# Kernel optimization log

Hardware: AMD Instinct MI355X
Metric: run time of the kernel (lower is better)

The kernel has to match this reference:

```python
import jax, jax.numpy as jnp
import numpy as np

N_HEADS = 8
N_LEVELS = 1
N_POINTS = 4
D_MODEL = 256
BATCH = 2
H0, W0 = 100, 150
LS = H0 * W0
LQ = 15000


def layer_norm(x, g, b, eps=1e-5):
    m = jnp.mean(x, -1, keepdims=True)
    v = jnp.var(x, -1, keepdims=True)
    return (x - m) * jax.lax.rsqrt(v + eps) * g + b


def bilinear_sample(v, Hl, Wl, loc):
    # v: [N, Hl*Wl, Hh, D] level features; loc in [0,1]: [N, Lq, Hh, P, 2] (x, y)
    Nb, _, Hh, D = v.shape
    Lq, P = loc.shape[1], loc.shape[3]
    x = loc[..., 0] * Wl - 0.5           # align_corners=False grid_sample convention
    y = loc[..., 1] * Hl - 0.5
    x0 = jnp.floor(x); y0 = jnp.floor(y)
    lx = (x - x0).transpose(0, 2, 1, 3)[..., None]   # [N,Hh,Lq,P,1]
    ly = (y - y0).transpose(0, 2, 1, 3)[..., None]
    x0i = x0.astype(jnp.int32); y0i = y0.astype(jnp.int32)
    vh = v.transpose(0, 2, 1, 3)                      # [N,Hh,Hl*Wl,D]

    def gather(xi, yi):
        valid = (xi >= 0) & (xi < Wl) & (yi >= 0) & (yi < Hl)   # zero padding
        idx = jnp.clip(yi, 0, Hl - 1) * Wl + jnp.clip(xi, 0, Wl - 1)
        idxf = idx.transpose(0, 2, 1, 3).reshape(Nb, Hh, Lq * P)
        g = jnp.take_along_axis(vh, idxf[..., None], axis=2).reshape(Nb, Hh, Lq, P, D)
        return g * valid.transpose(0, 2, 1, 3)[..., None]

    g00 = gather(x0i, y0i)
    g10 = gather(x0i + 1, y0i)
    g01 = gather(x0i, y0i + 1)
    g11 = gather(x0i + 1, y0i + 1)
    return (g00 * (1 - lx) * (1 - ly) + g10 * lx * (1 - ly)
            + g01 * (1 - lx) * ly + g11 * lx * ly)   # [N,Hh,Lq,P,D]


def ms_deform_attn(q, reference_points, src, shapes_np, starts_np, padding_mask,
                   W_val, b_val, W_off, b_off, W_attn, b_attn, W_out, b_out):
    Nb, Lq, C = q.shape
    Hh, D, L, P = N_HEADS, C // N_HEADS, N_LEVELS, N_POINTS
    value = src @ W_val + b_val
    value = jnp.where(padding_mask[..., None], 0.0, value).reshape(Nb, -1, Hh, D)
    offsets = (q @ W_off + b_off).reshape(Nb, Lq, Hh, L, P, 2)
    aw = jax.nn.softmax((q @ W_attn + b_attn).reshape(Nb, Lq, Hh, L * P), -1)
    aw = aw.reshape(Nb, Lq, Hh, L, P)
    # offset normalizer is (W, H) per level
    norm = jnp.asarray(shapes_np[:, ::-1].copy(), dtype=q.dtype)   # [L,2]
    loc = reference_points[:, :, None, :, None, :] + offsets / norm[None, None, None, :, None, :]
    out = 0.0
    for l in range(L):
        Hl, Wl = int(shapes_np[l, 0]), int(shapes_np[l, 1])
        s = int(starts_np[l])
        sampled = bilinear_sample(value[:, s:s + Hl * Wl], Hl, Wl, loc[:, :, :, l])
        out = out + jnp.sum(sampled * aw[:, :, :, l].transpose(0, 2, 1, 3)[..., None], axis=3)
    out = out.transpose(0, 2, 1, 3).reshape(Nb, Lq, C)
    return out @ W_out + b_out


def reference(tgt, query_pos, src_pos, tgt_spatial_shapes, reference_points,
              depth_reference_points, src, src_spatial_shapes, frame_start_index,
              src_padding_mask,
              W_dsa, b_dsa, g_nds, b_nds, W_off, b_off, W_attn, b_attn,
              W_val, b_val, W_out, b_out, W_csa, b_csa, g_n1, b_n1,
              W_ff, b_ff, g_n3, b_n3):
    ss = np.asarray(src_spatial_shapes)      # static level shapes
    starts = np.asarray(frame_start_index)
    # depth scale adaptation
    src_a = layer_norm(src @ W_dsa + b_dsa, g_nds, b_nds)
    q = tgt + query_pos
    tgt2 = ms_deform_attn(q, reference_points, src_a, ss, starts, src_padding_mask,
                          W_val, b_val, W_off, b_off, W_attn, b_attn, W_out, b_out)
    tgt2 = tgt2 @ W_csa + b_csa
    t = layer_norm(tgt + tgt2, g_n1, b_n1)
    # FFN: single linear d_model->d_model with exact GELU (per source code)
    ff = jax.nn.gelu(t @ W_ff + b_ff, approximate=False)
    return layer_norm(t + ff, g_n3, b_n3)


def setup_inputs() -> dict:
    key = jax.random.key(0)
    ks = jax.random.split(key, 24)
    C = D_MODEL
    Hh, L, P = N_HEADS, N_LEVELS, N_POINTS

    def lin(k, fin, fout, scale=None):
        s = (1.0 / np.sqrt(fin)) if scale is None else scale
        return (jax.random.normal(k, (fin, fout), jnp.float32) * s).astype(jnp.float32)

    inp = {}
    inp['tgt'] = jax.random.normal(ks[0], (BATCH, LQ, C), jnp.float32)
    inp['query_pos'] = 0.1 * jax.random.normal(ks[1], (BATCH, LQ, C), jnp.float32)
    inp['src_pos'] = 0.1 * jax.random.normal(ks[2], (BATCH, LS, C), jnp.float32)
    inp['tgt_spatial_shapes'] = jnp.array([[H0, W0]], jnp.int32)
    inp['reference_points'] = jax.random.uniform(ks[3], (BATCH, LQ, L, 2), jnp.float32)
    inp['depth_reference_points'] = jax.random.uniform(ks[4], (BATCH, LQ, 1, 2), jnp.float32)
    inp['src'] = jax.random.normal(ks[5], (BATCH, LS, C), jnp.float32)
    inp['src_spatial_shapes'] = jnp.array([[H0, W0]], jnp.int32)
    inp['frame_start_index'] = jnp.array([0], jnp.int32)
    inp['src_padding_mask'] = jnp.zeros((BATCH, LS), jnp.bool_)
    # parameters
    inp['W_dsa'] = lin(ks[6], C, C); inp['b_dsa'] = jnp.zeros((C,), jnp.float32)
    inp['g_nds'] = jnp.ones((C,), jnp.float32); inp['b_nds'] = jnp.zeros((C,), jnp.float32)
    inp['W_off'] = lin(ks[7], C, Hh * L * P * 2, scale=0.01)
    inp['b_off'] = 0.5 * jax.random.normal(ks[8], (Hh * L * P * 2,), jnp.float32)
    inp['W_attn'] = lin(ks[9], C, Hh * L * P)
    inp['b_attn'] = jnp.zeros((Hh * L * P,), jnp.float32)
    inp['W_val'] = lin(ks[10], C, C); inp['b_val'] = jnp.zeros((C,), jnp.float32)
    inp['W_out'] = lin(ks[11], C, C); inp['b_out'] = jnp.zeros((C,), jnp.float32)
    inp['W_csa'] = lin(ks[12], C, C); inp['b_csa'] = jnp.zeros((C,), jnp.float32)
    inp['g_n1'] = jnp.ones((C,), jnp.float32); inp['b_n1'] = jnp.zeros((C,), jnp.float32)
    inp['W_ff'] = lin(ks[13], C, C); inp['b_ff'] = jnp.zeros((C,), jnp.float32)
    inp['g_n3'] = jnp.ones((C,), jnp.float32); inp['b_n3'] = jnp.zeros((C,), jnp.float32)
    return inp
```

## Files before the change

### kernel.cpp

```cpp
#include <hip/hip_runtime.h>
#include <hip/hip_bf16.h>
#include <math.h>

#define LQ   15000
#define LS_  15000
#define NB   2
#define ROWS (NB*LQ)
#define HGT  100
#define WID  150

typedef __attribute__((ext_vector_type(8))) short bf16x8;
typedef __attribute__((ext_vector_type(4))) float f32x4;

__device__ inline short f2bf(float x) {
    __hip_bfloat16 h = __float2bfloat16(x);
    return *reinterpret_cast<short*>(&h);
}
__device__ inline unsigned pack2bf(float a, float b) {
    return ((unsigned)(unsigned short)f2bf(a)) | (((unsigned)(unsigned short)f2bf(b)) << 16);
}
__device__ inline float bf2f(short s) {
    return __uint_as_float(((unsigned)(unsigned short)s) << 16);
}
__device__ inline float gelu_exact(float x) {
    return 0.5f * x * (1.f + erff(x * 0.70710678118654752440f));
}

template<int MODE>
__global__ __launch_bounds__(256, 3) void fused2(
    const void* __restrict__ Ap,
    const short* __restrict__ W1T, const float* __restrict__ bias1,
    const float* __restrict__ res1,
    const float* __restrict__ g1v, const float* __restrict__ b1v,
    const short* __restrict__ W2T, const float* __restrict__ bias2,
    void* __restrict__ Out,
    const unsigned char* __restrict__ mask,
    const float* __restrict__ g2v, const float* __restrict__ b2v,
    int M)
{
    __shared__ __align__(16) char lds[54272];
    short (*Bs)[40]  = (short(*)[40])lds;
    short (*T)[264]  = (short(*)[264])(lds + 20480);
    short (*As)[40]  = (short(*)[40])(lds + 20480);

    const int tid = threadIdx.x;
    const int bm0 = blockIdx.x * 64;
    const int wave = tid >> 6, lane = tid & 63;
    const int quad = lane >> 4, c = lane & 15;

    f32x4 acc[16];
    #pragma unroll
    for (int t = 0; t < 16; ++t) acc[t] = (f32x4){0.f, 0.f, 0.f, 0.f};

    for (int k0 = 0; k0 < 256; k0 += 32) {
        if (MODE == 0) {
            const float* A = (const float*)Ap;
            #pragma unroll
            for (int it = 0; it < 2; ++it) {
                int f = it * 256 + tid; int m = f >> 3; int ko = (f & 7) * 4;
                int r = bm0 + m; if (r > M - 1) r = M - 1;
                float4 v = *(const float4*)&A[(size_t)r * 256 + k0 + ko];
                int2 p; p.x = pack2bf(v.x, v.y); p.y = pack2bf(v.z, v.w);
                *(int2*)&As[m][ko] = p;
            }
        } else {
            const short* A = (const short*)Ap;
            int m = tid >> 2; int ko = (tid & 3) * 8;
            int r = bm0 + m; if (r > M - 1) r = M - 1;
            *(int4*)&As[m][ko] = *(const int4*)&A[(size_t)r * 256 + k0 + ko];
        }
        #pragma unroll
        for (int it = 0; it < 4; ++it) {
            int f = it * 256 + tid; int n = f >> 2; int ko = (f & 3) * 8;
            *(int4*)&Bs[n][ko] = *(const int4*)&W1T[(size_t)n * 256 + k0 + ko];
        }
        __syncthreads();
        bf16x8 a = *(const bf16x8*)&As[wave * 16 + c][quad * 8];
        #pragma unroll
        for (int t = 0; t < 16; ++t) {
            bf16x8 b = *(const bf16x8*)&Bs[t * 16 + c][quad * 8];
            acc[t] = __builtin_amdgcn_mfma_f32_16x16x32_bf16(a, b, acc[t], 0, 0, 0);
        }
        __syncthreads();
    }

    {
        const int rb = wave * 16 + quad * 4;
        #pragma unroll
        for (int reg = 0; reg < 4; ++reg) {
            int rloc = rb + reg;
            int rg = bm0 + rloc; int rgl = (rg < M) ? rg : (M - 1);
            float s = 0.f, sq = 0.f;
            float vv[16];
            #pragma unroll
            for (int t = 0; t < 16; ++t) {
                int col = t * 16 + c;
                float v = acc[t][reg] + bias1[col];
                if (MODE == 1) v += res1[(size_t)rgl * 256 + col];
                vv[t] = v; s += v; sq += v * v;
            }
            #pragma unroll
            for (int o = 1; o < 16; o <<= 1) {
                s += __shfl_xor(s, o, 64); sq += __shfl_xor(sq, o, 64);
            }
            float mean = s * (1.f / 256.f);
            float var  = sq * (1.f / 256.f) - mean * mean;
            float rs   = rsqrtf(var + 1e-5f);
            #pragma unroll
            for (int t = 0; t < 16; ++t) {
                int col = t * 16 + c;
                T[rloc][col] = f2bf((vv[t] - mean) * rs * g1v[col] + b1v[col]);
            }
        }
    }

    #pragma unroll
    for (int t = 0; t < 16; ++t) acc[t] = (f32x4){0.f, 0.f, 0.f, 0.f};
    for (int k0 = 0; k0 < 256; k0 += 32) {
        #pragma unroll
        for (int it = 0; it < 4; ++it) {
            int f = it * 256 + tid; int n = f >> 2; int ko = (f & 3) * 8;
            *(int4*)&Bs[n][ko] = *(const int4*)&W2T[(size_t)n * 256 + k0 + ko];
        }
        __syncthreads();
        bf16x8 a = *(const bf16x8*)&T[wave * 16 + c][k0 + quad * 8];
        #pragma unroll
        for (int t = 0; t < 16; ++t) {
            bf16x8 b = *(const bf16x8*)&Bs[t * 16 + c][quad * 8];
            acc[t] = __builtin_amdgcn_mfma_f32_16x16x32_bf16(a, b, acc[t], 0, 0, 0);
        }
        __syncthreads();
    }

    const int rb = wave * 16 + quad * 4;
    if constexpr (MODE == 0) {
        short* O = (short*)Out;
        #pragma unroll
        for (int reg = 0; reg < 4; ++reg) {
            int rloc = rb + reg; int r = bm0 + rloc;
            if (r < M) {
                float mz = mask[r] ? 0.f : 1.f;
                int n = (r >= LS_) ? 1 : 0;
                int sidx = r - n * LS_;
                #pragma unroll
                for (int t = 0; t < 16; ++t) {
                    int col = t * 16 + c; int h = col >> 5, d = col & 31;
                    O[(((size_t)n * 8 + h) * LS_ + sidx) * 32 + d] =
                        f2bf((acc[t][reg] + bias2[col]) * mz);
                }
            }
        }
    } else {
        float* O = (float*)Out;
        #pragma unroll
        for (int reg = 0; reg < 4; ++reg) {
            int rloc = rb + reg; int r = bm0 + rloc;
            float s = 0.f, sq = 0.f;
            float vv[16];
            #pragma unroll
            for (int t = 0; t < 16; ++t) {
                int col = t * 16 + c;
                float v = gelu_exact(acc[t][reg] + bias2[col]) + bf2f(T[rloc][col]);
                vv[t] = v; s += v; sq += v * v;
            }
            #pragma unroll
            for (int o = 1; o < 16; o <<= 1) {
                s += __shfl_xor(s, o, 64); sq += __shfl_xor(sq, o, 64);
            }
            float mean = s * (1.f / 256.f);
            float var  = sq * (1.f / 256.f) - mean * mean;
            float rs   = rsqrtf(var + 1e-5f);
            if (r < M) {
                #pragma unroll
                for (int t = 0; t < 16; ++t) {
                    int col = t * 16 + c;
                    O[(size_t)r * 256 + col] = (vv[t] - mean) * rs * g2v[col] + b2v[col];
                }
            }
        }
    }
}

__global__ __launch_bounds__(256) void oa_gemm(
    const float* __restrict__ tgt, const float* __restrict__ qpos,
    const short* __restrict__ WToa, const float* __restrict__ b_oa,
    float* __restrict__ S_oa, int M)
{
    __shared__ short As[64][40];
    __shared__ short Bs[96][40];
    __shared__ float sb[96];

    const int tid = threadIdx.x;
    const int bm0 = blockIdx.x * 64;
    const int wave = tid >> 6, lane = tid & 63;
    const int quad = lane >> 4, c = lane & 15;

    if (tid < 96) sb[tid] = b_oa[tid];

    f32x4 acc[6];
    #pragma unroll
    for (int t = 0; t < 6; ++t) acc[t] = (f32x4){0.f, 0.f, 0.f, 0.f};

    for (int k0 = 0; k0 < 256; k0 += 32) {
        #pragma unroll
        for (int it = 0; it < 2; ++it) {
            int f = it * 256 + tid; int m = f >> 3; int ko = (f & 7) * 4;
            int r = bm0 + m; if (r > M - 1) r = M - 1;
            float4 v = *(const float4*)&tgt[(size_t)r * 256 + k0 + ko];
            float4 w = *(const float4*)&qpos[(size_t)r * 256 + k0 + ko];
            v.x += w.x; v.y += w.y; v.z += w.z; v.w += w.w;
            int2 p; p.x = pack2bf(v.x, v.y); p.y = pack2bf(v.z, v.w);
            *(int2*)&As[m][ko] = p;
        }
        {
            int f = tid;
            if (f < 192) {  }
            #pragma unroll
            for (int it = 0; it < 2; ++it) {
                int ff = it * 256 + tid;
                if (ff < 384) {
                    int n = ff >> 2; int ko = (ff & 3) * 8;
                    *(int4*)&Bs[n][ko] = *(const int4*)&WToa[(size_t)n * 256 + k0 + ko];
                }
            }
        }
        __syncthreads();
        bf16x8 a = *(const bf16x8*)&As[wave * 16 + c][quad * 8];
        #pragma unroll
        for (int t = 0; t < 6; ++t) {
            bf16x8 b = *(const bf16x8*)&Bs[t * 16 + c][quad * 8];
            acc[t] = __builtin_amdgcn_mfma_f32_16x16x32_bf16(a, b, acc[t], 0, 0, 0);
        }
        __syncthreads();
    }

    const int rb = wave * 16 + quad * 4;
    #pragma unroll
    for (int reg = 0; reg < 4; ++reg) {
        int r = bm0 + rb + reg;
        if (r < M) {
            #pragma unroll
            for (int t = 0; t < 6; ++t)
                S_oa[(size_t)r * 96 + t * 16 + c] = acc[t][reg] + sb[t * 16 + c];
        }
    }
}

__global__ __launch_bounds__(256) void deform_sample(
    const short* __restrict__ value,
    const float* __restrict__ S_oa,
    const float* __restrict__ refp,
    short* __restrict__ out)
{
    int grp = blockIdx.x * 32 + (threadIdx.x >> 3);
    int c4  = threadIdx.x & 7;
    int h = grp & 7;
    int r = grp >> 3;
    int n = (r >= LS_) ? 1 : 0;

    const float* row = S_oa + (size_t)r * 96;
    float rx = refp[(size_t)r * 2 + 0], ry = refp[(size_t)r * 2 + 1];
    float4 oA = *(const float4*)&row[h * 8];
    float4 oB = *(const float4*)&row[h * 8 + 4];
    float4 lg = *(const float4*)&row[64 + h * 4];

    float mx = fmaxf(fmaxf(lg.x, lg.y), fmaxf(lg.z, lg.w));
    float e0 = expf(lg.x - mx), e1 = expf(lg.y - mx), e2 = expf(lg.z - mx), e3 = expf(lg.w - mx);
    float inv = 1.f / (e0 + e1 + e2 + e3);
    float aw[4] = {e0 * inv, e1 * inv, e2 * inv, e3 * inv};
    float ox[4] = {oA.x, oA.z, oB.x, oB.z};
    float oy[4] = {oA.y, oA.w, oB.y, oB.w};

    const short* vb = value + (((size_t)n * 8 + h) * LS_) * 32 + c4 * 4;
    float a0 = 0.f, a1 = 0.f, a2 = 0.f, a3 = 0.f;

    #pragma unroll
    for (int p = 0; p < 4; ++p) {
        float x = rx * (float)WID + ox[p] - 0.5f;
        float y = ry * (float)HGT + oy[p] - 0.5f;
        float x0f = floorf(x), y0f = floorf(y);
        float lx = x - x0f, ly = y - y0f;
        int x0 = (int)x0f, y0 = (int)y0f;
        int x1 = x0 + 1, y1 = y0 + 1;
        bool vx0 = (x0 >= 0) & (x0 < WID), vx1 = (x1 >= 0) & (x1 < WID);
        bool vy0 = (y0 >= 0) & (y0 < HGT), vy1 = (y1 >= 0) & (y1 < HGT);
        float w00 = (vx0 & vy0) ? (1.f - lx) * (1.f - ly) * aw[p] : 0.f;
        float w10 = (vx1 & vy0) ? lx * (1.f - ly) * aw[p] : 0.f;
        float w01 = (vx0 & vy1) ? (1.f - lx) * ly * aw[p] : 0.f;
        float w11 = (vx1 & vy1) ? lx * ly * aw[p] : 0.f;
        int xc0 = min(max(x0, 0), WID - 1), xc1 = min(max(x1, 0), WID - 1);
        int yc0 = min(max(y0, 0), HGT - 1), yc1 = min(max(y1, 0), HGT - 1);
        int2 v00 = *(const int2*)&vb[(size_t)(yc0 * WID + xc0) * 32];
        int2 v10 = *(const int2*)&vb[(size_t)(yc0 * WID + xc1) * 32];
        int2 v01 = *(const int2*)&vb[(size_t)(yc1 * WID + xc0) * 32];
        int2 v11 = *(const int2*)&vb[(size_t)(yc1 * WID + xc1) * 32];
        a0 += w00 * __uint_as_float(((unsigned)v00.x) << 16)
            + w10 * __uint_as_float(((unsigned)v10.x) << 16)
            + w01 * __uint_as_float(((unsigned)v01.x) << 16)
            + w11 * __uint_as_float(((unsigned)v11.x) << 16);
        a1 += w00 * __uint_as_float(v00.x & 0xffff0000u)
            + w10 * __uint_as_float(v10.x & 0xffff0000u)
            + w01 * __uint_as_float(v01.x & 0xffff0000u)
            + w11 * __uint_as_float(v11.x & 0xffff0000u);
        a2 += w00 * __uint_as_float(((unsigned)v00.y) << 16)
            + w10 * __uint_as_float(((unsigned)v10.y) << 16)
            + w01 * __uint_as_float(((unsigned)v01.y) << 16)
            + w11 * __uint_as_float(((unsigned)v11.y) << 16);
        a3 += w00 * __uint_as_float(v00.y & 0xffff0000u)
            + w10 * __uint_as_float(v10.y & 0xffff0000u)
            + w01 * __uint_as_float(v01.y & 0xffff0000u)
            + w11 * __uint_as_float(v11.y & 0xffff0000u);
    }
    int2 o;
    o.x = pack2bf(a0, a1);
    o.y = pack2bf(a2, a3);
    *(int2*)&out[(size_t)r * 256 + h * 32 + c4 * 4] = o;
}

__global__ __launch_bounds__(256) void prep_all(
    const float* __restrict__ W_dsa, const float* __restrict__ W_val,
    const float* __restrict__ W_ff,  const float* __restrict__ W_out,
    const float* __restrict__ W_csa, const float* __restrict__ b_out,
    const float* __restrict__ b_csa, const float* __restrict__ W_off,
    const float* __restrict__ W_attn, const float* __restrict__ b_off,
    const float* __restrict__ b_attn,
    short* __restrict__ WT_dsa, short* __restrict__ WT_val, short* __restrict__ WT_ff,
    short* __restrict__ WT_c, float* __restrict__ bc,
    short* __restrict__ WT_oa, float* __restrict__ b_oa)
{
    __shared__ float tile[64][65];
    const int b = blockIdx.x, tid = threadIdx.x;
    if (b < 48) {
        const float* W = (b < 16) ? W_dsa : (b < 32) ? W_val : W_ff;
        short* WT = (b < 16) ? WT_dsa : (b < 32) ? WT_val : WT_ff;
        int t = b & 15; int bx = (t & 3) * 64, by = (t >> 2) * 64;
        #pragma unroll
        for (int it = 0; it < 4; ++it) {
            int f = it * 256 + tid; int i = f >> 4; int j = (f & 15) * 4;
            float4 v = *(const float4*)&W[(size_t)(by + i) * 256 + bx + j];
            tile[i][j] = v.x; tile[i][j + 1] = v.y; tile[i][j + 2] = v.z; tile[i][j + 3] = v.w;
        }
        __syncthreads();
        #pragma unroll
        for (int it = 0; it < 16; ++it) {
            int f = it * 256 + tid; int nl = f >> 6; int kl = f & 63;
            WT[(size_t)(bx + nl) * 256 + by + kl] = f2bf(tile[kl][nl]);
        }
    } else if (b < 304) {
        int k = b - 48, n = tid;
        float s = 0.f;
        #pragma unroll 8
        for (int j = 0; j < 256; ++j)
            s = fmaf(W_out[(size_t)k * 256 + j], W_csa[(size_t)j * 256 + n], s);
        WT_c[(size_t)n * 256 + k] = f2bf(s);
    } else if (b == 304) {
        int j = tid;
        float s = b_csa[j];
        #pragma unroll 8
        for (int k = 0; k < 256; ++k)
            s = fmaf(b_out[k], W_csa[(size_t)k * 256 + j], s);
        bc[j] = s;
    } else {
        int j = b - 305, k = tid;
        float v = (j < 64) ? W_off[(size_t)k * 64 + j] : W_attn[(size_t)k * 32 + (j - 64)];
        WT_oa[(size_t)j * 256 + k] = f2bf(v);
        if (k == 0) b_oa[j] = (j < 64) ? b_off[j] : b_attn[j - 64];
    }
}

extern "C" void kernel_launch(void* const* d_in, const int* in_sizes, int n_in,
                              void* d_out, int out_size, void* d_ws, size_t ws_size,
                              hipStream_t stream)
{
    const float* tgt       = (const float*)d_in[0];
    const float* query_pos = (const float*)d_in[1];
    const float* refp      = (const float*)d_in[4];
    const float* src       = (const float*)d_in[6];
    const unsigned char* mask = (const unsigned char*)d_in[9];
    const float* W_dsa  = (const float*)d_in[10]; const float* b_dsa  = (const float*)d_in[11];
    const float* g_nds  = (const float*)d_in[12]; const float* b_nds  = (const float*)d_in[13];
    const float* W_off  = (const float*)d_in[14]; const float* b_off  = (const float*)d_in[15];
    const float* W_attn = (const float*)d_in[16]; const float* b_attn = (const float*)d_in[17];
    const float* W_val  = (const float*)d_in[18]; const float* b_val  = (const float*)d_in[19];
    const float* W_out  = (const float*)d_in[20]; const float* b_out  = (const float*)d_in[21];
    const float* W_csa  = (const float*)d_in[22]; const float* b_csa  = (const float*)d_in[23];
    const float* g_n1   = (const float*)d_in[24]; const float* b_n1   = (const float*)d_in[25];
    const float* W_ff   = (const float*)d_in[26]; const float* b_ff   = (const float*)d_in[27];
    const float* g_n3   = (const float*)d_in[28]; const float* b_n3   = (const float*)d_in[29];
    float* out = (float*)d_out;

    short* attn_out = (short*)d_ws;
    short* value    = attn_out + (size_t)ROWS * 256;
    float* S_oa     = (float*)(value + (size_t)ROWS * 256);
    short* WT_dsa   = (short*)(S_oa + (size_t)ROWS * 96);
    short* WT_val   = WT_dsa + 65536;
    short* WT_ff    = WT_val + 65536;
    short* WT_c     = WT_ff + 65536;
    short* WT_oa    = WT_c + 65536;
    float* bc       = (float*)(WT_oa + 96 * 256);
    float* b_oa     = bc + 256;

    dim3 blk(256);
    const int GB = (ROWS + 63) / 64;

    prep_all<<<401, blk, 0, stream>>>(
        W_dsa, W_val, W_ff, W_out, W_csa, b_out, b_csa, W_off, W_attn, b_off, b_attn,
        WT_dsa, WT_val, WT_ff, WT_c, bc, WT_oa, b_oa);

    oa_gemm<<<GB, blk, 0, stream>>>(tgt, query_pos, WT_oa, b_oa, S_oa, ROWS);

    fused2<0><<<GB, blk, 0, stream>>>(
        src, WT_dsa, b_dsa, nullptr, g_nds, b_nds,
        WT_val, b_val, value, mask, nullptr, nullptr, ROWS);

    deform_sample<<<ROWS * 8 / 32, blk, 0, stream>>>(value, S_oa, refp, attn_out);

    fused2<1><<<GB, blk, 0, stream>>>(
        attn_out, WT_c, bc, tgt, g_n1, b_n1,
        WT_ff, b_ff, out, nullptr, g_n3, b_n3, ROWS);
}
```

Before: 332.8 us.

## Double-buffer weight tiles via direct global-to-LDS loads with swizzled layout

Rewrites the fused two-GEMM kernel's main loops. Weight tiles are now loaded straight from global memory into LDS with global_load_lds into two alternating buffers, so the next K-slice is fetched while the current one feeds the MFMAs. The activation row is kept in registers for the whole K range instead of being staged through LDS, and the LDS layout uses an XOR swizzle to avoid bank conflicts. The extra registers and the larger LDS footprint lower the occupancy hint from 3 to 2 blocks per CU.

```diff
diff --git a/kernel.cpp b/kernel.cpp
--- a/kernel.cpp
+++ b/kernel.cpp
@@ -26,8 +26,31 @@
     return 0.5f * x * (1.f + erff(x * 0.70710678118654752440f));
 }
 
+#if defined(__has_builtin)
+#if __has_builtin(__builtin_amdgcn_global_load_lds)
+#define HAS_GLL 1
+#endif
+#endif
+#ifndef HAS_GLL
+#define HAS_GLL 0
+#endif
+
+typedef unsigned int u32;
+
+__device__ __forceinline__ void gld_lds16(const void* g, void* l) {
+#if HAS_GLL
+    __builtin_amdgcn_global_load_lds(
+        (const __attribute__((address_space(1))) u32*)g,
+        (__attribute__((address_space(3))) u32*)l,
+        16, 0, 0);
+#else
+    int lane = threadIdx.x & 63;
+    *(int4*)((char*)l + lane * 16) = *(const int4*)g;
+#endif
+}
+
 template<int MODE>
-__global__ __launch_bounds__(256, 3) void fused2(
+__global__ __launch_bounds__(256, 2) void fused2(
     const void* __restrict__ Ap,
     const short* __restrict__ W1T, const float* __restrict__ bias1,
     const float* __restrict__ res1,
@@ -38,51 +61,75 @@
     const float* __restrict__ g2v, const float* __restrict__ b2v,
     int M)
 {
-    __shared__ __align__(16) char lds[54272];
-    short (*Bs)[40]  = (short(*)[40])lds;
-    short (*T)[264]  = (short(*)[264])(lds + 20480);
-    short (*As)[40]  = (short(*)[40])(lds + 20480);
+    __shared__ __align__(16) char lds[2 * 16384 + 64 * 264 * 2];
+    short (*T)[264] = (short(*)[264])(lds + 32768);
 
     const int tid = threadIdx.x;
     const int bm0 = blockIdx.x * 64;
     const int wave = tid >> 6, lane = tid & 63;
     const int quad = lane >> 4, c = lane & 15;
 
+    const int roff = c * 64 + ((quad ^ ((c >> 1) & 3)) << 4);
+
+    auto stageB = [&](int buf, const short* __restrict__ W, int k0) {
+        #pragma unroll
+        for (int it = 0; it < 4; ++it) {
+            int s = it * 256 + wave * 64 + lane;
+            int n = s >> 2;
+            int j = (s & 3) ^ ((n >> 1) & 3);
+            gld_lds16(W + (size_t)n * 256 + k0 + j * 8,
+                      lds + buf * 16384 + (it * 256 + wave * 64) * 16);
+        }
+    };
+
+    int rA = bm0 + wave * 16 + c; if (rA > M - 1) rA = M - 1;
+    bf16x8 aReg[8];
+
+    stageB(0, W1T, 0);
+
+    if (MODE == 1) {
+        const short* A = (const short*)Ap + (size_t)rA * 256 + quad * 8;
+        #pragma unroll
+        for (int k = 0; k < 8; ++k) aReg[k] = *(const bf16x8*)(A + k * 32);
+    } else {
+        const float* A = (const float*)Ap + (size_t)rA * 256 + quad * 8;
+        float4 lo[8], hi[8];
+        #pragma unroll
+        for (int k = 0; k < 8; ++k) {
+            lo[k] = *(const float4*)(A + k * 32);
+            hi[k] = *(const float4*)(A + k * 32 + 4);
+        }
+        #pragma unroll
+        for (int k = 0; k < 8; ++k) {
+            union { int4 i; bf16x8 v; } u;
+            u.i.x = pack2bf(lo[k].x, lo[k].y);
+            u.i.y = pack2bf(lo[k].z, lo[k].w);
+            u.i.z = pack2bf(hi[k].x, hi[k].y);
+            u.i.w = pack2bf(hi[k].z, hi[k].w);
+            aReg[k] = u.v;
+        }
+    }
+
     f32x4 acc[16];
     #pragma unroll
     for (int t = 0; t < 16; ++t) acc[t] = (f32x4){0.f, 0.f, 0.f, 0.f};
 
-    for (int k0 = 0; k0 < 256; k0 += 32) {
-        if (MODE == 0) {
-            const float* A = (const float*)Ap;
-            #pragma unroll
-            for (int it = 0; it < 2; ++it) {
-                int f = it * 256 + tid; int m = f >> 3; int ko = (f & 7) * 4;
-                int r = bm0 + m; if (r > M - 1) r = M - 1;
-                float4 v = *(const float4*)&A[(size_t)r * 256 + k0 + ko];
-                int2 p; p.x = pack2bf(v.x, v.y); p.y = pack2bf(v.z, v.w);
-                *(int2*)&As[m][ko] = p;
-            }
-        } else {
-            const short* A = (const short*)Ap;
-            int m = tid >> 2; int ko = (tid & 3) * 8;
-            int r = bm0 + m; if (r > M - 1) r = M - 1;
-            *(int4*)&As[m][ko] = *(const int4*)&A[(size_t)r * 256 + k0 + ko];
-        }
-        #pragma unroll
-        for (int it = 0; it < 4; ++it) {
-            int f = it * 256 + tid; int n = f >> 2; int ko = (f & 3) * 8;
-            *(int4*)&Bs[n][ko] = *(const int4*)&W1T[(size_t)n * 256 + k0 + ko];
+    __syncthreads();
+
+    #pragma unroll
+    for (int k0c = 0; k0c < 8; ++k0c) {
+        if (k0c < 7) stageB((k0c + 1) & 1, W1T, (k0c + 1) * 32);
+        const char* bb = lds + (k0c & 1) * 16384 + roff;
+        bf16x8 a = aReg[k0c];
+        #pragma unroll
+        for (int t = 0; t < 16; ++t) {
+            bf16x8 b = *(const bf16x8*)(bb + t * 1024);
+            acc[t] = __builtin_amdgcn_mfma_f32_16x16x32_bf16(a, b, acc[t], 0, 0, 0);
         }
         __syncthreads();
-        bf16x8 a = *(const bf16x8*)&As[wave * 16 + c][quad * 8];
-        #pragma unroll
-        for (int t = 0; t < 16; ++t) {
-            bf16x8 b = *(const bf16x8*)&Bs[t * 16 + c][quad * 8];
-            acc[t] = __builtin_amdgcn_mfma_f32_16x16x32_bf16(a, b, acc[t], 0, 0, 0);
-        }
-        __syncthreads();
-    }
+    }
+
+    stageB(0, W2T, 0);
 
     {
         const int rb = wave * 16 + quad * 4;
@@ -115,18 +162,22 @@
     }
 
     #pragma unroll
+    for (int k = 0; k < 8; ++k)
+        aReg[k] = *(const bf16x8*)&T[wave * 16 + c][k * 32 + quad * 8];
+
+    #pragma unroll
     for (int t = 0; t < 16; ++t) acc[t] = (f32x4){0.f, 0.f, 0.f, 0.f};
-    for (int k0 = 0; k0 < 256; k0 += 32) {
-        #pragma unroll
-        for (int it = 0; it < 4; ++it) {
-            int f = it * 256 + tid; int n = f >> 2; int ko = (f & 3) * 8;
-            *(int4*)&Bs[n][ko] = *(const int4*)&W2T[(size_t)n * 256 + k0 + ko];
-        }
-        __syncthreads();
-        bf16x8 a = *(const bf16x8*)&T[wave * 16 + c][k0 + quad * 8];
+
+    __syncthreads();
+
+    #pragma unroll
+    for (int k0c = 0; k0c < 8; ++k0c) {
+        if (k0c < 7) stageB((k0c + 1) & 1, W2T, (k0c + 1) * 32);
+        const char* bb = lds + (k0c & 1) * 16384 + roff;
+        bf16x8 a = aReg[k0c];
         #pragma unroll
         for (int t = 0; t < 16; ++t) {
-            bf16x8 b = *(const bf16x8*)&Bs[t * 16 + c][quad * 8];
+            bf16x8 b = *(const bf16x8*)(bb + t * 1024);
             acc[t] = __builtin_amdgcn_mfma_f32_16x16x32_bf16(a, b, acc[t], 0, 0, 0);
         }
         __syncthreads();
@@ -213,8 +264,6 @@
             *(int2*)&As[m][ko] = p;
         }
         {
-            int f = tid;
-            if (f < 192) {  }
             #pragma unroll
             for (int it = 0; it < 2; ++it) {
                 int ff = it * 256 + tid;
```

Measured after the change: 293.7 us. 1.13x faster.
